# Kernel tuning notes

Hardware: AMD Instinct MI355X
Metric: run time of the kernel (lower is better)

The kernel has to match this reference:

```python
import jax, jax.numpy as jnp
import numpy as np

B, N, TS, TT, C, H, L = 64, 128, 48, 12, 3, 128, 2


def _u(key, shape, fan):
    s = 1.0 / np.sqrt(fan)
    return jax.random.uniform(key, shape, jnp.float32, -s, s)


def setup_inputs() -> dict:
    key = jax.random.key(0)
    ks = jax.random.split(key, 24)
    return {
        'flow_x': jax.random.normal(ks[0], (B, N, TS, C), jnp.float32),
        'flow_y': jax.random.normal(ks[1], (B, N, TT, C), jnp.float32),
        'enc_w_ih0': _u(ks[2], (3 * H, C), H),
        'enc_w_ih1': _u(ks[3], (3 * H, H), H),
        'enc_w_hh': _u(ks[4], (L, 3 * H, H), H),
        'enc_b_ih': _u(ks[5], (L, 3 * H), H),
        'enc_b_hh': _u(ks[6], (L, 3 * H), H),
        'enc_hid_w': _u(ks[7], (H, H), H),
        'enc_hid_b': _u(ks[8], (H,), H),
        'dec_w_ih0': _u(ks[9], (3 * H, C + H), H),
        'dec_w_ih1': _u(ks[10], (3 * H, H), H),
        'dec_w_hh': _u(ks[11], (L, 3 * H, H), H),
        'dec_b_ih': _u(ks[12], (L, 3 * H), H),
        'dec_b_hh': _u(ks[13], (L, 3 * H), H),
        'attn_w': _u(ks[14], (H, 2 * H), 2 * H),
        'attn_b': _u(ks[15], (H,), 2 * H),
        'v_w': _u(ks[16], (1, H), H),
        'fc_w': _u(ks[17], (C, 2 * H + C), 2 * H + C),
        'fc_b': _u(ks[18], (C,), 2 * H + C),
    }


def gru_cell(x, h, w_ih, w_hh, b_ih, b_hh):
    gi = x @ w_ih.T + b_ih  # [NB, 3H]
    gh = h @ w_hh.T + b_hh
    ir, iz, i_n = jnp.split(gi, 3, axis=-1)
    hr, hz, h_n = jnp.split(gh, 3, axis=-1)
    r = jax.nn.sigmoid(ir + hr)
    z = jax.nn.sigmoid(iz + hz)
    n = jnp.tanh(i_n + r * h_n)
    return (1.0 - z) * n + z * h


def run_gru_layer(xs, h0, w_ih, w_hh, b_ih, b_hh):
    def step(h, x):
        hn = gru_cell(x, h, w_ih, w_hh, b_ih, b_hh)
        return hn, hn
    hT, ys = jax.lax.scan(step, h0, xs)
    return ys, hT


def reference(flow_x, flow_y, enc_w_ih0, enc_w_ih1, enc_w_hh, enc_b_ih, enc_b_hh,
              enc_hid_w, enc_hid_b, dec_w_ih0, dec_w_ih1, dec_w_hh, dec_b_ih,
              dec_b_hh, attn_w, attn_b, v_w, fc_w, fc_b):
    b, n, tt, c = flow_y.shape
    ts = flow_x.shape[2]
    h = enc_hid_w.shape[0]
    nb = n * b
    # fuse (node, batch) -> one batch dim: [TS, N*B, C]
    xs = flow_x.transpose(2, 1, 0, 3).reshape(ts, nb, c)
    h0 = jnp.zeros((nb, h), flow_x.dtype)
    # encoder: 2-layer GRU
    ys0, hT0 = run_gru_layer(xs, h0, enc_w_ih0, enc_w_hh[0], enc_b_ih[0], enc_b_hh[0])
    en_out, hT1 = run_gru_layer(ys0, h0, enc_w_ih1, enc_w_hh[1], enc_b_ih[1], enc_b_hh[1])
    hidden = jnp.tanh(jnp.stack([hT0, hT1]) @ enc_hid_w.T + enc_hid_b)  # [L, NB, H]
    dec_in0 = xs[-1]  # last source step, [NB, C]

    def dec_step(carry, _):
        hid, dec_in = carry
        h_last = hid[1]  # [NB, H]
        # attention over encoder timesteps
        cat = jnp.concatenate(
            [jnp.broadcast_to(h_last, (ts, nb, h)), en_out], axis=-1)  # [TS, NB, 2H]
        energy = jnp.tanh(cat @ attn_w.T + attn_b)
        scores = jnp.squeeze(energy @ v_w.T, -1)  # [TS, NB]
        a = jax.nn.softmax(scores, axis=0)
        context = jnp.einsum('tb,tbh->bh', a, en_out)  # [NB, H]
        x0 = jnp.concatenate([dec_in, context], axis=-1)  # [NB, C+H]
        h0n = gru_cell(x0, hid[0], dec_w_ih0, dec_w_hh[0], dec_b_ih[0], dec_b_hh[0])
        h1n = gru_cell(h0n, hid[1], dec_w_ih1, dec_w_hh[1], dec_b_ih[1], dec_b_hh[1])
        # de_output == hidden[-1] after step, so fc input is [h1n, h1n, dec_in]
        out = jnp.concatenate([h1n, h1n, dec_in], axis=-1) @ fc_w.T + fc_b  # [NB, C]
        return (jnp.stack([h0n, h1n]), out), out

    _, outs = jax.lax.scan(dec_step, (hidden, dec_in0), None, length=tt)
    pred = outs.reshape(tt, n, b, c).transpose(2, 1, 0, 3)  # [B, N, TT, C]
    return pred, flow_y
```

## Files before the change

### kernel.cpp

```cpp
#include <hip/hip_runtime.h>
#include <hip/hip_bf16.h>
#include <math.h>

#define NB   8192
#define TSRC 48
#define TTGT 12
#define ROWS 32
#define DR   16

typedef float f32x4 __attribute__((ext_vector_type(4)));
typedef float f32x2 __attribute__((ext_vector_type(2)));
typedef short bf16x8 __attribute__((ext_vector_type(8)));
typedef short bf16x4 __attribute__((ext_vector_type(4)));
typedef unsigned u32x2 __attribute__((ext_vector_type(2)));

#define QSCALE 2.8853900817779268f

__device__ __forceinline__ float bf2f(unsigned short u){ return __uint_as_float(((unsigned)u)<<16); }
__device__ __forceinline__ unsigned short f2bf(float f){
  unsigned u = __float_as_uint(f);
  u += 0x7fffu + ((u>>16)&1u);
  return (unsigned short)(u>>16);
}
__device__ __forceinline__ float sigm(float x){ return 1.0f/(1.0f+__expf(-x)); }
__device__ __forceinline__ float tanhfast(float x){
  float a = fminf(fabsf(x), 15.0f);
  float e = __expf(2.0f*a);
  float r = 1.0f - 2.0f/(e+1.0f);
  return copysignf(r, x);
}
__device__ __forceinline__ f32x4 mfma16(bf16x8 a, bf16x8 b, f32x4 c){
  return __builtin_amdgcn_mfma_f32_16x16x32_bf16(a,b,c,0,0,0);
}
__device__ __forceinline__ bf16x8 ldsfrag(const short* buf, int lr, int kbase, int koff){
  const int el = (kbase + koff) ^ ((lr&7)<<3);
  return *(const bf16x8*)(buf + lr*128 + el);
}
__device__ __forceinline__ uint2 enc8_fp8(bf16x8 v){
  int t0 = __builtin_amdgcn_cvt_pk_fp8_f32(bf2f((unsigned short)v[0]), bf2f((unsigned short)v[1]), 0, false);
  t0     = __builtin_amdgcn_cvt_pk_fp8_f32(bf2f((unsigned short)v[2]), bf2f((unsigned short)v[3]), t0, true);
  int t1 = __builtin_amdgcn_cvt_pk_fp8_f32(bf2f((unsigned short)v[4]), bf2f((unsigned short)v[5]), 0, false);
  t1     = __builtin_amdgcn_cvt_pk_fp8_f32(bf2f((unsigned short)v[6]), bf2f((unsigned short)v[7]), t1, true);
  uint2 o; o.x = (unsigned)t0; o.y = (unsigned)t1; return o;
}
__device__ __forceinline__ void dec4_fp8(unsigned u, float* out){
  f32x2 lo = __builtin_amdgcn_cvt_pk_f32_fp8((int)u, false);
  f32x2 hi = __builtin_amdgcn_cvt_pk_f32_fp8((int)u, true);
  out[0]=lo.x; out[1]=lo.y; out[2]=hi.x; out[3]=hi.y;
}
__device__ __forceinline__ uint2 ntload_u2(const unsigned char* p){
  u32x2 v = __builtin_nontemporal_load((const u32x2*)p);
  uint2 o; o.x = v.x; o.y = v.y; return o;
}
__device__ __forceinline__ unsigned ntload_u1(const unsigned char* p){
  return __builtin_nontemporal_load((const unsigned*)p);
}

__global__ __launch_bounds__(512,2) void enc_mega(
  const float* __restrict__ xs3,
  const unsigned short* __restrict__ Wc0, const unsigned short* __restrict__ Wc1,
  const unsigned short* __restrict__ Wp,
  const float* __restrict__ bih, const float* __restrict__ bhh,
  const float* __restrict__ attn_b,
  unsigned char* __restrict__ en_s, unsigned char* __restrict__ p_s,
  float* __restrict__ hseed0, float* __restrict__ hseed1)
{
  __shared__ float h0f[ROWS][132];
  __shared__ float h1f[ROWS][132];
  __shared__ short h0b[ROWS][128];
  __shared__ short h1b[ROWS][128];
  __shared__ short xfrag[TSRC][ROWS][8];
  __shared__ short ptile[ROWS][128];

  const int bid  = blockIdx.x;
  const int row0 = bid*ROWS;
  const int tid  = threadIdx.x;
  const int lane = tid & 63;
  const int w    = tid >> 6;
  const int l15  = lane & 15;
  const int q4   = lane >> 4;
  const int koff = q4*8;
  const int jcol = w*16 + l15;

  for (int e=tid; e<ROWS*132; e+=512){ int r=e/132, c=e%132; h0f[r][c]=0.f; h1f[r][c]=0.f; }
  for (int e=tid; e<ROWS*128; e+=512){ ((short*)h0b)[e]=0; ((short*)h1b)[e]=0; }
  for (int e=tid; e<TSRC*ROWS; e+=512){
    int t = e/ROWS, r = e%ROWS;
    const float* s = xs3 + ((size_t)t*NB + row0 + r)*3;
    short* d = &xfrag[t][r][0];
    d[0]=(short)f2bf(s[0]); d[1]=(short)f2bf(s[1]); d[2]=(short)f2bf(s[2]);
    d[3]=0; d[4]=0; d[5]=0; d[6]=0; d[7]=0;
  }

  bf16x8 wb0[5][3], wb1[8][3], wp[4];
  #pragma unroll
  for (int g=0; g<3; g++){
    #pragma unroll
    for (int ks=0; ks<5; ks++)
      wb0[ks][g] = *(const bf16x8*)(Wc0 + (size_t)(g*128 + jcol)*160 + ks*32 + koff);
    #pragma unroll
    for (int ks=0; ks<8; ks++)
      wb1[ks][g] = *(const bf16x8*)(Wc1 + (size_t)(g*128 + jcol)*256 + ks*32 + koff);
  }
  #pragma unroll
  for (int ks=0; ks<4; ks++)
    wp[ks] = *(const bf16x8*)(Wp + (size_t)jcol*128 + ks*32 + koff);

  const float bR0 = bih[jcol]     + bhh[jcol];
  const float bZ0 = bih[128+jcol] + bhh[128+jcol];
  const float bNi0= bih[256+jcol];
  const float bNh0= bhh[256+jcol];
  const float bR1 = bih[384+jcol]     + bhh[384+jcol];
  const float bZ1 = bih[384+128+jcol] + bhh[384+128+jcol];
  const float bNi1= bih[384+256+jcol];
  const float bNh1= bhh[384+256+jcol];
  const float pb  = attn_b[jcol];
  const bf16x8 zz = {0,0,0,0,0,0,0,0};
  const f32x4 z4 = {0.f,0.f,0.f,0.f};

  __syncthreads();

  for (int t=0; t<TSRC; t++){
    f32x4 aR[2],aZ[2],aNh[2],aNi[2];
    #pragma unroll
    for (int m=0;m<2;m++){ aR[m]=z4; aZ[m]=z4; aNh[m]=z4; aNi[m]=z4; }
    #pragma unroll
    for (int m=0;m<2;m++){
      const int lr = m*16 + l15;
      #pragma unroll
      for (int ks=0;ks<4;ks++){
        bf16x8 a = ldsfrag(&h0b[0][0], lr, ks*32, koff);
        aR[m]=mfma16(a,wb0[ks][0],aR[m]);
        aZ[m]=mfma16(a,wb0[ks][1],aZ[m]);
        aNh[m]=mfma16(a,wb0[ks][2],aNh[m]);
      }
      bf16x8 ax = zz;
      if (q4==0) ax = *(const bf16x8*)(&xfrag[t][lr][0]);
      aR[m]=mfma16(ax,wb0[4][0],aR[m]);
      aZ[m]=mfma16(ax,wb0[4][1],aZ[m]);
      aNi[m]=mfma16(ax,wb0[4][2],aNi[m]);
    }
    __syncthreads();
    #pragma unroll
    for (int m=0;m<2;m++){
      #pragma unroll
      for (int rr=0;rr<4;rr++){
        int r = m*16 + q4*4 + rr;
        float rg = sigm(aR[m][rr]+bR0);
        float zgg= sigm(aZ[m][rr]+bZ0);
        float ng = tanhfast(aNi[m][rr]+bNi0 + rg*(aNh[m][rr]+bNh0));
        float hn = (1.f-zgg)*ng + zgg*h0f[r][jcol];
        h0f[r][jcol] = hn;
        h0b[r][jcol ^ ((r&7)<<3)] = (short)f2bf(hn);
      }
    }
    __syncthreads();
    #pragma unroll
    for (int m=0;m<2;m++){ aR[m]=z4; aZ[m]=z4; aNh[m]=z4; aNi[m]=z4; }
    #pragma unroll
    for (int m=0;m<2;m++){
      const int lr = m*16 + l15;
      #pragma unroll
      for (int ks=0;ks<4;ks++){
        bf16x8 a = ldsfrag(&h1b[0][0], lr, ks*32, koff);
        aR[m]=mfma16(a,wb1[ks][0],aR[m]);
        aZ[m]=mfma16(a,wb1[ks][1],aZ[m]);
        aNh[m]=mfma16(a,wb1[ks][2],aNh[m]);
      }
      #pragma unroll
      for (int ks=0;ks<4;ks++){
        bf16x8 a = ldsfrag(&h0b[0][0], lr, ks*32, koff);
        aR[m]=mfma16(a,wb1[4+ks][0],aR[m]);
        aZ[m]=mfma16(a,wb1[4+ks][1],aZ[m]);
        aNi[m]=mfma16(a,wb1[4+ks][2],aNi[m]);
      }
    }
    __syncthreads();
    #pragma unroll
    for (int m=0;m<2;m++){
      #pragma unroll
      for (int rr=0;rr<4;rr++){
        int r = m*16 + q4*4 + rr;
        float rg = sigm(aR[m][rr]+bR1);
        float zgg= sigm(aZ[m][rr]+bZ1);
        float ng = tanhfast(aNi[m][rr]+bNi1 + rg*(aNh[m][rr]+bNh1));
        float hn = (1.f-zgg)*ng + zgg*h1f[r][jcol];
        h1f[r][jcol] = hn;
        h1b[r][jcol ^ ((r&7)<<3)] = (short)f2bf(hn);
      }
    }
    __syncthreads();
    f32x4 pacc[2]; pacc[0]=z4; pacc[1]=z4;
    #pragma unroll
    for (int m=0;m<2;m++){
      const int lr = m*16 + l15;
      #pragma unroll
      for (int ks=0;ks<4;ks++){
        bf16x8 a = ldsfrag(&h1b[0][0], lr, ks*32, koff);
        pacc[m]=mfma16(a,wp[ks],pacc[m]);
      }
    }
    #pragma unroll
    for (int m=0;m<2;m++){
      #pragma unroll
      for (int rr=0;rr<4;rr++){
        int r = m*16 + q4*4 + rr;
        ptile[r][jcol] = (short)f2bf((pacc[m][rr] + pb) * QSCALE);
      }
    }
    __syncthreads();
    {
      const int r = tid >> 4, jc = tid & 15, j0 = jc*8;
      bf16x8 ev = *(const bf16x8*)(&h1b[r][j0 ^ ((r&7)<<3)]);
      bf16x8 pv = *(const bf16x8*)(&ptile[r][j0]);
      const size_t base = ((((size_t)bid*TSRC + t)*ROWS + r)<<7) + j0;
      *(uint2*)(en_s + base) = enc8_fp8(ev);
      *(uint2*)(p_s  + base) = enc8_fp8(pv);
    }
  }
  for (int e=tid; e<ROWS*128; e+=512){
    int r = e>>7, c = e&127;
    hseed0[(size_t)(row0+r)*128 + c] = h0f[r][c];
    hseed1[(size_t)(row0+r)*128 + c] = h1f[r][c];
  }
}

__global__ __launch_bounds__(512,4) void dec_mega(
  const float* __restrict__ hseed0, const float* __restrict__ hseed1,
  const unsigned short* __restrict__ Ehw, const float* __restrict__ ehb,
  const float* __restrict__ xs3,
  const unsigned short* __restrict__ Wd0, const unsigned short* __restrict__ Wd1,
  const unsigned short* __restrict__ Wq, const float* __restrict__ v_w,
  const float* __restrict__ bih, const float* __restrict__ bhh,
  const unsigned char* __restrict__ en_s, const unsigned char* __restrict__ p_s,
  const float* __restrict__ fcs, const float* __restrict__ ftail,
  float* __restrict__ pred)
{
  __shared__ short hd0b[DR][128];
  __shared__ short hd1b[DR][128];
  __shared__ float qf[DR][132];
  __shared__ float s_lds[TSRC*DR];
  __shared__ short ctxb[DR][128];
  __shared__ float din[DR][4];
  __shared__ float vls[128];

  const int db   = blockIdx.x;
  const int row0 = db*DR;
  const int tid  = threadIdx.x;
  const int lane = tid & 63;
  const int w    = tid >> 6;
  const int l15  = lane & 15;
  const int q4   = lane >> 4;
  const int koff = q4*8;
  const int jcol = w*16 + l15;
  const f32x4 z4 = {0.f,0.f,0.f,0.f};
  const bf16x8 zz = {0,0,0,0,0,0,0,0};
  const size_t sb0 = (size_t)(db>>1)*TSRC*4096 + (size_t)(db&1)*2048;

  if (tid < 128) vls[tid] = v_w[tid];
  if (tid < DR){
    const float* s = xs3 + ((size_t)(TSRC-1)*NB + row0 + tid)*3;
    din[tid][0]=s[0]; din[tid][1]=s[1]; din[tid][2]=s[2];
  }

  float h0reg[4], h1reg[4];

  {
    const float bb = ehb[jcol];
    #pragma unroll
    for (int L=0; L<2; L++){
      const float* hs = L ? hseed1 : hseed0;
      f32x4 acc = z4;
      #pragma unroll
      for (int ks=0;ks<4;ks++){
        const float* ap = hs + (size_t)(row0+l15)*128 + ks*32 + koff;
        float4 f0 = *(const float4*)(ap);
        float4 f1 = *(const float4*)(ap+4);
        bf16x8 a;
        a[0]=(short)f2bf(f0.x); a[1]=(short)f2bf(f0.y); a[2]=(short)f2bf(f0.z); a[3]=(short)f2bf(f0.w);
        a[4]=(short)f2bf(f1.x); a[5]=(short)f2bf(f1.y); a[6]=(short)f2bf(f1.z); a[7]=(short)f2bf(f1.w);
        bf16x8 b = *(const bf16x8*)(Ehw + (size_t)jcol*128 + ks*32 + koff);
        acc = mfma16(a,b,acc);
      }
      #pragma unroll
      for (int rr=0;rr<4;rr++){
        int r = q4*4 + rr;
        float v = tanhfast(acc[rr] + bb);
        if (L) h1reg[rr] = v; else h0reg[rr] = v;
        short hb = (short)f2bf(v);
        if (L) hd1b[r][jcol ^ ((r&7)<<3)] = hb;
        else   hd0b[r][jcol ^ ((r&7)<<3)] = hb;
      }
    }
  }

  const float bR0 = bih[jcol]     + bhh[jcol];
  const float bZ0 = bih[128+jcol] + bhh[128+jcol];
  const float bNi0= bih[256+jcol];
  const float bNh0= bhh[256+jcol];
  const float bR1 = bih[384+jcol]     + bhh[384+jcol];
  const float bZ1 = bih[384+128+jcol] + bhh[384+128+jcol];
  const float bNi1= bih[384+256+jcol];
  const float bNh1= bhh[384+256+jcol];

  __syncthreads();

  const int jr = l15*8;
  float vreg[8]; float Vpart = 0.f;
  #pragma unroll
  for (int e=0;e<8;e++){ vreg[e] = vls[jr+e]; Vpart += vreg[e]; }

  for (int t=0; t<TTGT; t++){
    {
      f32x4 qa = z4;
      #pragma unroll
      for (int ks=0;ks<4;ks++){
        bf16x8 a = ldsfrag(&hd1b[0][0], l15, ks*32, koff);
        bf16x8 b = *(const bf16x8*)(Wq + (size_t)jcol*128 + ks*32 + koff);
        qa = mfma16(a,b,qa);
      }
      #pragma unroll
      for (int rr=0;rr<4;rr++)
        qf[q4*4+rr][jcol] = qa[rr] * QSCALE;
    }
    __syncthreads();
    {
      int sidx = w*96 + q4;
      const unsigned char* pp = p_s + sb0;
      uint2 pv = ntload_u2(pp + (size_t)(sidx>>4)*4096 + (sidx&15)*128 + jr);
      #pragma unroll 4
      for (int k=0;k<24;k++){
        int snext = sidx + 4;
        uint2 pn = pv;
        if (k < 23)
          pn = ntload_u2(pp + (size_t)(snext>>4)*4096 + (snext&15)*128 + jr);
        const int r = sidx & 15;
        const float4 q0 = *(const float4*)(&qf[r][jr]);
        const float4 q1 = *(const float4*)(&qf[r][jr+4]);
        float pd[8];
        dec4_fp8(pv.x, pd); dec4_fp8(pv.y, pd+4);
        float s2 = 0.f;
        s2 = fmaf(vreg[0], __builtin_amdgcn_rcpf(__builtin_amdgcn_exp2f(pd[0]+q0.x)+1.f), s2);
        s2 = fmaf(vreg[1], __builtin_amdgcn_rcpf(__builtin_amdgcn_exp2f(pd[1]+q0.y)+1.f), s2);
        s2 = fmaf(vreg[2], __builtin_amdgcn_rcpf(__builtin_amdgcn_exp2f(pd[2]+q0.z)+1.f), s2);
        s2 = fmaf(vreg[3], __builtin_amdgcn_rcpf(__builtin_amdgcn_exp2f(pd[3]+q0.w)+1.f), s2);
        s2 = fmaf(vreg[4], __builtin_amdgcn_rcpf(__builtin_amdgcn_exp2f(pd[4]+q1.x)+1.f), s2);
        s2 = fmaf(vreg[5], __builtin_amdgcn_rcpf(__builtin_amdgcn_exp2f(pd[5]+q1.y)+1.f), s2);
        s2 = fmaf(vreg[6], __builtin_amdgcn_rcpf(__builtin_amdgcn_exp2f(pd[6]+q1.z)+1.f), s2);
        s2 = fmaf(vreg[7], __builtin_amdgcn_rcpf(__builtin_amdgcn_exp2f(pd[7]+q1.w)+1.f), s2);
        float sl = Vpart - 2.f*s2;
        sl += __shfl_xor(sl, 1); sl += __shfl_xor(sl, 2);
        sl += __shfl_xor(sl, 4); sl += __shfl_xor(sl, 8);
        if (l15 == 0) s_lds[sidx] = sl;
        sidx = snext; pv = pn;
      }
    }
    __syncthreads();
    if (tid < DR){
      float sv[TSRC]; float mx = -1e30f;
      #pragma unroll
      for (int k=0;k<TSRC;k++){ sv[k] = s_lds[k*DR+tid]; mx = fmaxf(mx, sv[k]); }
      float den = 0.f;
      #pragma unroll
      for (int k=0;k<TSRC;k++){ float e2 = __expf(sv[k]-mx); sv[k]=e2; den += e2; }
      float rd = 1.0f/den;
      #pragma unroll
      for (int k=0;k<TSRC;k++) s_lds[k*DR+tid] = sv[k]*rd;
    }
    __syncthreads();
    {
      const int cr = 2*w + (lane>>5);
      const int cj = (lane&31)*4;
      const unsigned char* ep = en_s + sb0 + cr*128 + cj;
      float ca0=0.f, ca1=0.f, ca2=0.f, ca3=0.f;
      #pragma unroll 3
      for (int tt=0; tt<TSRC; tt+=4){
        unsigned u0 = ntload_u1(ep + (size_t)(tt  )*4096);
        unsigned u1 = ntload_u1(ep + (size_t)(tt+1)*4096);
        unsigned u2 = ntload_u1(ep + (size_t)(tt+2)*4096);
        unsigned u3 = ntload_u1(ep + (size_t)(tt+3)*4096);
        float a0 = s_lds[(tt  )*DR + cr];
        float a1 = s_lds[(tt+1)*DR + cr];
        float a2 = s_lds[(tt+2)*DR + cr];
        float a3 = s_lds[(tt+3)*DR + cr];
        float d0[4], d1[4], d2[4], d3[4];
        dec4_fp8(u0,d0); dec4_fp8(u1,d1); dec4_fp8(u2,d2); dec4_fp8(u3,d3);
        ca0 += a0*d0[0] + a1*d1[0] + a2*d2[0] + a3*d3[0];
        ca1 += a0*d0[1] + a1*d1[1] + a2*d2[1] + a3*d3[1];
        ca2 += a0*d0[2] + a1*d1[2] + a2*d2[2] + a3*d3[2];
        ca3 += a0*d0[3] + a1*d1[3] + a2*d2[3] + a3*d3[3];
      }
      bf16x4 cv;
      cv[0]=(short)f2bf(ca0); cv[1]=(short)f2bf(ca1);
      cv[2]=(short)f2bf(ca2); cv[3]=(short)f2bf(ca3);
      *(bf16x4*)(&ctxb[cr][cj ^ ((cr&7)<<3)]) = cv;
    }
    __syncthreads();
    {
      f32x4 aR=z4, aZ=z4, aNh=z4, aNi=z4;
      #pragma unroll
      for (int ks=0; ks<9; ks++){
        bf16x8 b0 = *(const bf16x8*)(Wd0 + (size_t)(jcol)*288     + ks*32 + koff);
        bf16x8 b1 = *(const bf16x8*)(Wd0 + (size_t)(128+jcol)*288 + ks*32 + koff);
        bf16x8 b2 = *(const bf16x8*)(Wd0 + (size_t)(256+jcol)*288 + ks*32 + koff);
        bf16x8 a;
        if (ks < 4)       a = ldsfrag(&hd0b[0][0], l15, ks*32, koff);
        else if (ks == 4){
          a = zz;
          if (q4==0){ a[0]=(short)f2bf(din[l15][0]); a[1]=(short)f2bf(din[l15][1]); a[2]=(short)f2bf(din[l15][2]); }
        } else            a = ldsfrag(&ctxb[0][0], l15, (ks-5)*32, koff);
        aR = mfma16(a,b0,aR);
        aZ = mfma16(a,b1,aZ);
        if (ks<4) aNh = mfma16(a,b2,aNh);
        else      aNi = mfma16(a,b2,aNi);
      }
      __syncthreads();
      #pragma unroll
      for (int rr=0;rr<4;rr++){
        int r = q4*4 + rr;
        float rg = sigm(aR[rr]+bR0);
        float zg = sigm(aZ[rr]+bZ0);
        float ng = tanhfast(aNi[rr]+bNi0 + rg*(aNh[rr]+bNh0));
        float hn = (1.f-zg)*ng + zg*h0reg[rr];
        h0reg[rr] = hn;
        hd0b[r][jcol ^ ((r&7)<<3)] = (short)f2bf(hn);
      }
    }
    __syncthreads();
    {
      f32x4 aR=z4, aZ=z4, aNh=z4, aNi=z4;
      #pragma unroll
      for (int ks=0; ks<8; ks++){
        bf16x8 b0 = *(const bf16x8*)(Wd1 + (size_t)(jcol)*256     + ks*32 + koff);
        bf16x8 b1 = *(const bf16x8*)(Wd1 + (size_t)(128+jcol)*256 + ks*32 + koff);
        bf16x8 b2 = *(const bf16x8*)(Wd1 + (size_t)(256+jcol)*256 + ks*32 + koff);
        bf16x8 a = (ks<4) ? ldsfrag(&hd1b[0][0], l15, ks*32, koff)
                          : ldsfrag(&hd0b[0][0], l15, (ks-4)*32, koff);
        aR = mfma16(a,b0,aR);
        aZ = mfma16(a,b1,aZ);
        if (ks<4) aNh = mfma16(a,b2,aNh);
        else      aNi = mfma16(a,b2,aNi);
      }
      __syncthreads();
      #pragma unroll
      for (int rr=0;rr<4;rr++){
        int r = q4*4 + rr;
        float rg = sigm(aR[rr]+bR1);
        float zg = sigm(aZ[rr]+bZ1);
        float ng = tanhfast(aNi[rr]+bNi1 + rg*(aNh[rr]+bNh1));
        float hn = (1.f-zg)*ng + zg*h1reg[rr];
        h1reg[rr] = hn;
        hd1b[r][jcol ^ ((r&7)<<3)] = (short)f2bf(hn);
      }
    }
    __syncthreads();
    if (tid < 16*DR){
      const int fr = tid >> 4, fu = tid & 15, fj0 = fu*8;
      bf16x8 hv8 = *(const bf16x8*)(&hd1b[fr][fj0 ^ ((fr&7)<<3)]);
      float hv[8];
      #pragma unroll
      for (int e=0;e<8;e++) hv[e] = bf2f((unsigned short)hv8[e]);
      float o0=0.f,o1=0.f,o2=0.f;
      {
        float4 wa = *(const float4*)(fcs + fj0);
        float4 wb = *(const float4*)(fcs + fj0 + 4);
        o0 = wa.x*hv[0]+wa.y*hv[1]+wa.z*hv[2]+wa.w*hv[3]
           + wb.x*hv[4]+wb.y*hv[5]+wb.z*hv[6]+wb.w*hv[7];
      }
      {
        float4 wa = *(const float4*)(fcs + 132 + fj0);
        float4 wb = *(const float4*)(fcs + 132 + fj0 + 4);
        o1 = wa.x*hv[0]+wa.y*hv[1]+wa.z*hv[2]+wa.w*hv[3]
           + wb.x*hv[4]+wb.y*hv[5]+wb.z*hv[6]+wb.w*hv[7];
      }
      {
        float4 wa = *(const float4*)(fcs + 264 + fj0);
        float4 wb = *(const float4*)(fcs + 264 + fj0 + 4);
        o2 = wa.x*hv[0]+wa.y*hv[1]+wa.z*hv[2]+wa.w*hv[3]
           + wb.x*hv[4]+wb.y*hv[5]+wb.z*hv[6]+wb.w*hv[7];
      }
      #pragma unroll
      for (int off=1; off<16; off<<=1){
        o0 += __shfl_xor(o0, off);
        o1 += __shfl_xor(o1, off);
        o2 += __shfl_xor(o2, off);
      }
      if (fu == 0){
        float d0 = din[fr][0], d1 = din[fr][1], d2 = din[fr][2];
        o0 += ftail[3]  + ftail[0]*d0 + ftail[1]*d1 + ftail[2]*d2;
        o1 += ftail[7]  + ftail[4]*d0 + ftail[5]*d1 + ftail[6]*d2;
        o2 += ftail[11] + ftail[8]*d0 + ftail[9]*d1 + ftail[10]*d2;
        const int nb = row0 + fr;
        const int n = nb >> 6, b = nb & 63;
        float* pr = pred + ((size_t)(b*128 + n)*TTGT + t)*3;
        __builtin_nontemporal_store(o0, pr);
        __builtin_nontemporal_store(o1, pr+1);
        __builtin_nontemporal_store(o2, pr+2);
        din[fr][0]=o0; din[fr][1]=o1; din[fr][2]=o2;
      }
    }
    __syncthreads();
  }
}

__global__ __launch_bounds__(256) void build_kernel(
  const float* __restrict__ e_ih0, const float* __restrict__ e_ih1,
  const float* __restrict__ e_hh,
  const float* __restrict__ d_ih0, const float* __restrict__ d_ih1,
  const float* __restrict__ d_hh,
  const float* __restrict__ attn_w, const float* __restrict__ ehw_f,
  const float* __restrict__ fc_w, const float* __restrict__ fc_b,
  unsigned short* __restrict__ Wc_e0, unsigned short* __restrict__ Wc_e1,
  unsigned short* __restrict__ Wc_d0, unsigned short* __restrict__ Wc_d1,
  unsigned short* __restrict__ Wq, unsigned short* __restrict__ Wp,
  unsigned short* __restrict__ Ehw,
  float* __restrict__ fcs, float* __restrict__ ftail)
{
  int idx = blockIdx.x*256 + threadIdx.x;
  if (idx >= 418200) return;
  if (idx < 61440){
    int j = idx/160, k = idx%160;
    float v = (k<128) ? e_hh[(size_t)j*128 + k]
            : (k<131) ? e_ih0[j*3 + (k-128)] : 0.0f;
    Wc_e0[idx] = f2bf(v);
  } else if (idx < 159744){
    int i = idx - 61440; int j = i/256, k = i%256;
    float v = (k<128) ? e_hh[(size_t)(384 + j)*128 + k]
                      : e_ih1[(size_t)j*128 + (k-128)];
    Wc_e1[i] = f2bf(v);
  } else if (idx < 270336){
    int i = idx - 159744; int j = i/288, k = i%288;
    float v = (k<128) ? d_hh[(size_t)j*128 + k]
            : (k<131) ? d_ih0[(size_t)j*131 + (k-128)]
            : (k<160) ? 0.0f
                      : d_ih0[(size_t)j*131 + 3 + (k-160)];
    Wc_d0[i] = f2bf(v);
  } else if (idx < 368640){
    int i = idx - 270336; int j = i/256, k = i%256;
    float v = (k<128) ? d_hh[(size_t)(384 + j)*128 + k]
                      : d_ih1[(size_t)j*128 + (k-128)];
    Wc_d1[i] = f2bf(v);
  } else if (idx < 385024){
    int i = idx - 368640; int j = i/128, k = i%128;
    Wq[i] = f2bf(attn_w[(size_t)j*256 + k]);
  } else if (idx < 401408){
    int i = idx - 385024; int j = i/128, k = i%128;
    Wp[i] = f2bf(attn_w[(size_t)j*256 + 128 + k]);
  } else if (idx < 417792){
    int i = idx - 401408;
    Ehw[i] = f2bf(ehw_f[i]);
  } else if (idx < 418188){
    int i = idx - 417792; int g = i/132, j = i%132;
    fcs[i] = (j<128) ? (fc_w[(size_t)g*259 + j] + fc_w[(size_t)g*259 + 128 + j]) : 0.0f;
  } else {
    int i = idx - 418188; int g = i/4, e = i%4;
    ftail[i] = (e<3) ? fc_w[(size_t)g*259 + 256 + e] : fc_b[g];
  }
}

__global__ __launch_bounds__(256) void pack_kernel(
  const float* __restrict__ fx, float* __restrict__ xs3)
{
  int idx = blockIdx.x*256 + threadIdx.x;
  if (idx >= TSRC*NB) return;
  int nb = idx & (NB-1), t = idx >> 13;
  int n = nb >> 6, b = nb & 63;
  const float* s = fx + (((size_t)(b*128) + n)*TSRC + t)*3;
  float* d = xs3 + (size_t)idx*3;
  d[0]=s[0]; d[1]=s[1]; d[2]=s[2];
}

extern "C" void kernel_launch(void* const* d_in, const int* in_sizes, int n_in,
                              void* d_out, int out_size, void* d_ws, size_t ws_size,
                              hipStream_t stream)
{
  const float* flow_x   = (const float*)d_in[0];
  const float* flow_y   = (const float*)d_in[1];
  const float* enc_w_ih0= (const float*)d_in[2];
  const float* enc_w_ih1= (const float*)d_in[3];
  const float* enc_w_hh = (const float*)d_in[4];
  const float* enc_b_ih = (const float*)d_in[5];
  const float* enc_b_hh = (const float*)d_in[6];
  const float* enc_hid_w= (const float*)d_in[7];
  const float* enc_hid_b= (const float*)d_in[8];
  const float* dec_w_ih0= (const float*)d_in[9];
  const float* dec_w_ih1= (const float*)d_in[10];
  const float* dec_w_hh = (const float*)d_in[11];
  const float* dec_b_ih = (const float*)d_in[12];
  const float* dec_b_hh = (const float*)d_in[13];
  const float* attn_w   = (const float*)d_in[14];
  const float* attn_b   = (const float*)d_in[15];
  const float* v_w      = (const float*)d_in[16];
  const float* fc_w     = (const float*)d_in[17];
  const float* fc_b     = (const float*)d_in[18];

  float* out_pred = (float*)d_out;
  float* out_fy   = out_pred + (size_t)64*128*TTGT*3;

  char* ws = (char*)d_ws;
  size_t off = 0;
  auto alloc = [&](size_t bytes)->void* {
    void* pp = ws + off; off += (bytes + 255) & ~(size_t)255; return pp;
  };
  float*          xs3    = (float*)alloc((size_t)TSRC*NB*3*4);
  unsigned char*  en_s   = (unsigned char*)alloc((size_t)TSRC*NB*128);
  unsigned char*  p_s    = (unsigned char*)alloc((size_t)TSRC*NB*128);
  float*          hseed0 = (float*)alloc((size_t)NB*128*4);
  float*          hseed1 = (float*)alloc((size_t)NB*128*4);
  unsigned short* Wc_e0  = (unsigned short*)alloc((size_t)384*160*2);
  unsigned short* Wc_e1  = (unsigned short*)alloc((size_t)384*256*2);
  unsigned short* Wc_d0  = (unsigned short*)alloc((size_t)384*288*2);
  unsigned short* Wc_d1  = (unsigned short*)alloc((size_t)384*256*2);
  unsigned short* attnWq = (unsigned short*)alloc((size_t)128*128*2);
  unsigned short* attnWp = (unsigned short*)alloc((size_t)128*128*2);
  unsigned short* Ehw    = (unsigned short*)alloc((size_t)128*128*2);
  float*          fcs    = (float*)alloc((size_t)3*132*4);
  float*          ftail  = (float*)alloc((size_t)12*4);

  hipMemcpyAsync(out_fy, flow_y, (size_t)64*128*TTGT*3*4,
                 hipMemcpyDeviceToDevice, stream);
  build_kernel<<<1634, 256, 0, stream>>>(
      enc_w_ih0, enc_w_ih1, enc_w_hh, dec_w_ih0, dec_w_ih1, dec_w_hh,
      attn_w, enc_hid_w, fc_w, fc_b,
      Wc_e0, Wc_e1, Wc_d0, Wc_d1, attnWq, attnWp, Ehw, fcs, ftail);
  pack_kernel<<<1536, 256, 0, stream>>>(flow_x, xs3);

  enc_mega<<<NB/ROWS, 512, 0, stream>>>(
      xs3, Wc_e0, Wc_e1, attnWp, enc_b_ih, enc_b_hh, attn_b,
      en_s, p_s, hseed0, hseed1);

  dec_mega<<<NB/DR, 512, 0, stream>>>(
      hseed0, hseed1, Ehw, enc_hid_b, xs3, Wc_d0, Wc_d1, attnWq, v_w,
      dec_b_ih, dec_b_hh, en_s, p_s, fcs, ftail, out_pred);
}
```

Baseline: 1.163 ms.

## Parallelize decoder softmax across waves and store attention buffers in bf16

The attention softmax moves from 16 threads each looping serially over 48 source steps to a wave-per-row form, where each lane holds one step and max and sum use shuffle reductions. The query and score/probability shared buffers also change from fp32 to bf16, which cuts LDS footprint and may raise occupancy or cut LDS traffic. The cost is lower precision in scores and attention weights, plus extra conversion instructions in the hot energy loop.

```diff
diff --git a/kernel.cpp b/kernel.cpp
--- a/kernel.cpp
+++ b/kernel.cpp
@@ -238,8 +238,8 @@
 {
   __shared__ short hd0b[DR][128];
   __shared__ short hd1b[DR][128];
-  __shared__ float qf[DR][132];
-  __shared__ float s_lds[TSRC*DR];
+  __shared__ unsigned short qfb[DR][128];
+  __shared__ unsigned short s16[TSRC*DR];
   __shared__ short ctxb[DR][128];
   __shared__ float din[DR][4];
   __shared__ float vls[128];
@@ -321,7 +321,7 @@
       }
       #pragma unroll
       for (int rr=0;rr<4;rr++)
-        qf[q4*4+rr][jcol] = qa[rr] * QSCALE;
+        qfb[q4*4+rr][jcol] = f2bf(qa[rr] * QSCALE);
     }
     __syncthreads();
     {
@@ -335,37 +335,40 @@
         if (k < 23)
           pn = ntload_u2(pp + (size_t)(snext>>4)*4096 + (snext&15)*128 + jr);
         const int r = sidx & 15;
-        const float4 q0 = *(const float4*)(&qf[r][jr]);
-        const float4 q1 = *(const float4*)(&qf[r][jr+4]);
+        bf16x8 qv = *(const bf16x8*)(&qfb[r][jr]);
         float pd[8];
         dec4_fp8(pv.x, pd); dec4_fp8(pv.y, pd+4);
         float s2 = 0.f;
-        s2 = fmaf(vreg[0], __builtin_amdgcn_rcpf(__builtin_amdgcn_exp2f(pd[0]+q0.x)+1.f), s2);
-        s2 = fmaf(vreg[1], __builtin_amdgcn_rcpf(__builtin_amdgcn_exp2f(pd[1]+q0.y)+1.f), s2);
-        s2 = fmaf(vreg[2], __builtin_amdgcn_rcpf(__builtin_amdgcn_exp2f(pd[2]+q0.z)+1.f), s2);
-        s2 = fmaf(vreg[3], __builtin_amdgcn_rcpf(__builtin_amdgcn_exp2f(pd[3]+q0.w)+1.f), s2);
-        s2 = fmaf(vreg[4], __builtin_amdgcn_rcpf(__builtin_amdgcn_exp2f(pd[4]+q1.x)+1.f), s2);
-        s2 = fmaf(vreg[5], __builtin_amdgcn_rcpf(__builtin_amdgcn_exp2f(pd[5]+q1.y)+1.f), s2);
-        s2 = fmaf(vreg[6], __builtin_amdgcn_rcpf(__builtin_amdgcn_exp2f(pd[6]+q1.z)+1.f), s2);
-        s2 = fmaf(vreg[7], __builtin_amdgcn_rcpf(__builtin_amdgcn_exp2f(pd[7]+q1.w)+1.f), s2);
+        s2 = fmaf(vreg[0], __builtin_amdgcn_rcpf(__builtin_amdgcn_exp2f(pd[0]+bf2f((unsigned short)qv[0]))+1.f), s2);
+        s2 = fmaf(vreg[1], __builtin_amdgcn_rcpf(__builtin_amdgcn_exp2f(pd[1]+bf2f((unsigned short)qv[1]))+1.f), s2);
+        s2 = fmaf(vreg[2], __builtin_amdgcn_rcpf(__builtin_amdgcn_exp2f(pd[2]+bf2f((unsigned short)qv[2]))+1.f), s2);
+        s2 = fmaf(vreg[3], __builtin_amdgcn_rcpf(__builtin_amdgcn_exp2f(pd[3]+bf2f((unsigned short)qv[3]))+1.f), s2);
+        s2 = fmaf(vreg[4], __builtin_amdgcn_rcpf(__builtin_amdgcn_exp2f(pd[4]+bf2f((unsigned short)qv[4]))+1.f), s2);
+        s2 = fmaf(vreg[5], __builtin_amdgcn_rcpf(__builtin_amdgcn_exp2f(pd[5]+bf2f((unsigned short)qv[5]))+1.f), s2);
+        s2 = fmaf(vreg[6], __builtin_amdgcn_rcpf(__builtin_amdgcn_exp2f(pd[6]+bf2f((unsigned short)qv[6]))+1.f), s2);
+        s2 = fmaf(vreg[7], __builtin_amdgcn_rcpf(__builtin_amdgcn_exp2f(pd[7]+bf2f((unsigned short)qv[7]))+1.f), s2);
         float sl = Vpart - 2.f*s2;
         sl += __shfl_xor(sl, 1); sl += __shfl_xor(sl, 2);
         sl += __shfl_xor(sl, 4); sl += __shfl_xor(sl, 8);
-        if (l15 == 0) s_lds[sidx] = sl;
+        if (l15 == 0) s16[sidx] = f2bf(sl);
         sidx = snext; pv = pn;
       }
     }
     __syncthreads();
-    if (tid < DR){
-      float sv[TSRC]; float mx = -1e30f;
-      #pragma unroll
-      for (int k=0;k<TSRC;k++){ sv[k] = s_lds[k*DR+tid]; mx = fmaxf(mx, sv[k]); }
-      float den = 0.f;
-      #pragma unroll
-      for (int k=0;k<TSRC;k++){ float e2 = __expf(sv[k]-mx); sv[k]=e2; den += e2; }
-      float rd = 1.0f/den;
-      #pragma unroll
-      for (int k=0;k<TSRC;k++) s_lds[k*DR+tid] = sv[k]*rd;
+    {
+      #pragma unroll
+      for (int h=0; h<2; h++){
+        const int r = w + h*8;
+        float s = (lane < TSRC) ? bf2f(s16[lane*DR + r]) : -1e30f;
+        float mx = s;
+        #pragma unroll
+        for (int off=32; off>=1; off>>=1) mx = fmaxf(mx, __shfl_xor(mx, off));
+        float e2 = (lane < TSRC) ? __expf(s - mx) : 0.f;
+        float den = e2;
+        #pragma unroll
+        for (int off=32; off>=1; off>>=1) den += __shfl_xor(den, off);
+        if (lane < TSRC) s16[lane*DR + r] = f2bf(e2 / den);
+      }
     }
     __syncthreads();
     {
@@ -379,10 +382,10 @@
         unsigned u1 = ntload_u1(ep + (size_t)(tt+1)*4096);
         unsigned u2 = ntload_u1(ep + (size_t)(tt+2)*4096);
         unsigned u3 = ntload_u1(ep + (size_t)(tt+3)*4096);
-        float a0 = s_lds[(tt  )*DR + cr];
-        float a1 = s_lds[(tt+1)*DR + cr];
-        float a2 = s_lds[(tt+2)*DR + cr];
-        float a3 = s_lds[(tt+3)*DR + cr];
+        float a0 = bf2f(s16[(tt  )*DR + cr]);
+        float a1 = bf2f(s16[(tt+1)*DR + cr]);
+        float a2 = bf2f(s16[(tt+2)*DR + cr]);
+        float a3 = bf2f(s16[(tt+3)*DR + cr]);
         float d0[4], d1[4], d2[4], d3[4];
         dec4_fp8(u0,d0); dec4_fp8(u1,d1); dec4_fp8(u2,d2); dec4_fp8(u3,d3);
         ca0 += a0*d0[0] + a1*d1[0] + a2*d2[0] + a3*d3[0];
```

New measurement: 1.106 ms (median of 2 runs). -4.9%, faster.
